# Optimization experiments

Hardware: AMD Instinct MI355X
Metric: run time of the kernel (lower is better)

Reference implementation:

```python
import jax, jax.numpy as jnp
import numpy as np

N, E, R, D = 100000, 600000, 3, 128  # nodes, edges per relation, relations, hidden


def setup_inputs() -> dict:
    key = jax.random.key(0)
    ks = jax.random.split(key, 12)
    sc = 1.0 / np.sqrt(D)
    return dict(
        x=jax.random.normal(ks[0], (N, D), jnp.float32),
        edge_src=jax.random.randint(ks[1], (R, E), 0, N, jnp.int32),
        edge_dst=jax.random.randint(ks[2], (R, E), 0, N, jnp.int32),
        edge_w=jax.random.uniform(ks[3], (R, E), jnp.float32),
        W=jax.random.normal(ks[4], (R, D, D), jnp.float32) * sc,
        attn_l=jax.random.normal(ks[5], (R, D), jnp.float32) * sc,
        attn_r=jax.random.normal(ks[6], (R, D), jnp.float32) * sc,
        gat_b=jnp.zeros((R, D), jnp.float32),
        bi_w=jax.random.normal(ks[7], (D, D), jnp.float32) * sc,
        bi_b=jnp.zeros((D,), jnp.float32),
        si_w=jax.random.normal(ks[8], (D, D), jnp.float32) * sc,
        si_b=jnp.zeros((D,), jnp.float32),
        res_w=jax.random.normal(ks[9], (), jnp.float32),
        ln_g=jnp.ones((D,), jnp.float32),
        ln_b=jnp.zeros((D,), jnp.float32),
    )


def _leaky(x, slope):
    return jnp.where(x >= 0, x, slope * x)


def _gat(x, W, al, ar, b, src, dst, ew):
    # DGL GATConv, 1 head, edge-weighted: h = xW; e = LReLU(a_l.h_src + a_r.h_dst);
    # alpha = edge_softmax(e per dst) * edge_weight; out[d] = sum alpha * h_src + bias.
    h = x @ W                                   # (N, D)
    el = (h * al).sum(-1)                       # (N,)
    er = (h * ar).sum(-1)                       # (N,)
    e = _leaky(el[src] + er[dst], 0.2)          # (E,)
    m = jax.ops.segment_max(e, dst, num_segments=N)
    a = jnp.exp(e - m[dst])
    s = jax.ops.segment_sum(a, dst, num_segments=N)
    alpha = a / s[dst] * ew                     # (E,)
    out = jax.ops.segment_sum(alpha[:, None] * h[src], dst, num_segments=N)
    return out + b                              # zero-indegree nodes -> bias only


def reference(x, edge_src, edge_dst, edge_w, W, attn_l, attn_r, gat_b,
              bi_w, bi_b, si_w, si_b, res_w, ln_g, ln_b):
    # per-relation intra aggregation, stacked along relation axis: (N, R, D)
    feats = jnp.stack(
        [_gat(x, W[r], attn_l[r], attn_r[r], gat_b[r],
              edge_src[r], edge_dst[r], edge_w[r]) for r in range(R)], axis=1)
    # FM-style bi-interaction over the relation axis
    s = feats.sum(axis=1)                       # (N, D)
    deep_fm = 0.5 * (s ** 2 - (feats ** 2).sum(axis=1))
    nfm = _leaky(deep_fm @ bi_w.T + bi_b, 0.01) + _leaky(s @ si_w.T + si_b, 0.01)
    # gated residual + LayerNorm
    out = nfm + x * jax.nn.sigmoid(res_w)
    mu = out.mean(-1, keepdims=True)
    var = ((out - mu) ** 2).mean(-1, keepdims=True)
    return (out - mu) * jax.lax.rsqrt(var + 1e-5) * ln_g + ln_b
```

## Files before the change

### kernel.cpp

```cpp
#include <hip/hip_runtime.h>

#define DD 128
typedef unsigned int u32;
typedef __attribute__((ext_vector_type(8))) short bf16x8;
typedef __attribute__((ext_vector_type(4))) float f32x4;

__device__ __forceinline__ float lrelu(float v, float s) { return v >= 0.f ? v : s * v; }
__device__ __forceinline__ ushort f2bf(float f) {
  union { float f; u32 u; } v; v.f = f;
  u32 u = v.u;
  return (ushort)((u + 0x7FFFu + ((u >> 16) & 1u)) >> 16);
}

union frag_cvt { uint4 u; bf16x8 h; };

__global__ __launch_bounds__(256) void k_prep_w(const float* __restrict__ W,
                                                short* __restrict__ WA)
{
  int t = blockIdx.x * 256 + threadIdx.x;
  int lane = t & 63, ks = (t >> 6) & 3, cf = (t >> 8) & 7, r = t >> 11;
  int c = cf * 16 + (lane & 15);
  int kb = ks * 32 + (lane >> 4) * 8;
  const float* Wr = W + (size_t)r * DD * DD;
  ushort o[8];
#pragma unroll
  for (int j = 0; j < 8; j++) o[j] = f2bf(Wr[(size_t)(kb + j) * DD + c]);
  uint4 st;
  st.x = (u32)o[0] | ((u32)o[1] << 16);
  st.y = (u32)o[2] | ((u32)o[3] << 16);
  st.z = (u32)o[4] | ((u32)o[5] << 16);
  st.w = (u32)o[6] | ((u32)o[7] << 16);
  *(uint4*)(WA + (size_t)t * 8) = st;
}

__global__ __launch_bounds__(256) void k_prep_cw(const float* __restrict__ bw,
                                                 const float* __restrict__ sw,
                                                 short* __restrict__ WB)
{
  int t = blockIdx.x * 256 + threadIdx.x;
  int lane = t & 63, ks = (t >> 6) & 3, cf = (t >> 8) & 7, m = t >> 11;
  const float* src = m ? sw : bw;
  int c = cf * 16 + (lane & 15);
  int k = ks * 32 + (lane >> 4) * 8;
  const float* pr = src + (size_t)c * DD + k;
  uint4 st;
  st.x = (u32)f2bf(pr[0]) | ((u32)f2bf(pr[1]) << 16);
  st.y = (u32)f2bf(pr[2]) | ((u32)f2bf(pr[3]) << 16);
  st.z = (u32)f2bf(pr[4]) | ((u32)f2bf(pr[5]) << 16);
  st.w = (u32)f2bf(pr[6]) | ((u32)f2bf(pr[7]) << 16);
  *(uint4*)(WB + (size_t)t * 8) = st;
}

__global__ void k_prep_av(const float* __restrict__ W, const float* __restrict__ al,
                          const float* __restrict__ ar, float* __restrict__ wl,
                          float* __restrict__ wr)
{
  int t = blockIdx.x * 192 + threadIdx.x;
  if (t >= 384) return;
  int r = t >> 7, k = t & 127;
  const float* Wrow = W + (size_t)r * DD * DD + (size_t)k * DD;
  const float* alr = al + r * DD;
  const float* arr = ar + r * DD;
  float pl = 0.f, pr = 0.f;
  for (int c = 0; c < DD; c++) { float w = Wrow[c]; pl = fmaf(w, alr[c], pl); pr = fmaf(w, arr[c], pr); }
  wl[t] = pl; wr[t] = pr;
}

__global__ __launch_bounds__(256) void k_prep_xrow(
    const float* __restrict__ x, const float* __restrict__ wl, const float* __restrict__ wr,
    u32* __restrict__ xrow, float* __restrict__ el, int2* __restrict__ bex, int N)
{
  const int wid = (int)(((long long)blockIdx.x * 256 + threadIdx.x) >> 6);
  const int lane = threadIdx.x & 63;
  if (wid >= N) return;
  float2 xv = *(const float2*)(x + (size_t)wid * DD + lane * 2);
  xrow[(size_t)wid * 64 + lane] = (u32)f2bf(xv.x) | ((u32)f2bf(xv.y) << 16);
  float d[6];
#pragma unroll
  for (int r = 0; r < 3; r++) {
    float2 wlv = *(const float2*)(wl + r * DD + lane * 2);
    float2 wrv = *(const float2*)(wr + r * DD + lane * 2);
    d[r]     = xv.x * wlv.x + xv.y * wlv.y;
    d[r + 3] = xv.x * wrv.x + xv.y * wrv.y;
  }
#pragma unroll
  for (int o = 32; o; o >>= 1) {
#pragma unroll
    for (int k = 0; k < 6; k++) d[k] += __shfl_xor(d[k], o);
  }
  if (lane == 0) {
#pragma unroll
    for (int r = 0; r < 3; r++) {
      el[(size_t)r * N + wid] = d[r];
      bex[(size_t)r * N + wid].y = __float_as_int(d[r + 3]);
    }
  }
}

__global__ void k_hist3(const int* __restrict__ dst, int* __restrict__ cnt,
                        int* __restrict__ rank, int N, int E) {
  int i = blockIdx.x * 256 + threadIdx.x;
  int r = blockIdx.y;
  if (i < E) {
    size_t ei = (size_t)r * E + i;
    rank[ei] = atomicAdd(cnt + (size_t)r * N + dst[ei], 1);
  }
}

__global__ __launch_bounds__(256) void k_scan_bsum(const int* __restrict__ cnt,
                                                   int* __restrict__ bsum, int M)
{
  __shared__ int red[256];
  const int t = threadIdx.x;
  const int g0 = blockIdx.x * 2048 + t * 8;
  int s = 0;
#pragma unroll
  for (int j = 0; j < 8; j++) { int i = g0 + j; if (i < M) s += cnt[i]; }
  red[t] = s;
  __syncthreads();
  for (int o = 128; o; o >>= 1) {
    if (t < o) red[t] += red[t + o];
    __syncthreads();
  }
  if (t == 0) bsum[blockIdx.x] = red[0];
}

__global__ __launch_bounds__(256) void k_scan_btop(const int* __restrict__ bsum,
                                                   int* __restrict__ bpre, int NB)
{
  __shared__ int sums[256];
  const int t = threadIdx.x;
  int v = (t < NB) ? bsum[t] : 0;
  sums[t] = v;
  __syncthreads();
  for (int o = 1; o < 256; o <<= 1) {
    int u = (t >= o) ? sums[t - o] : 0;
    __syncthreads();
    sums[t] += u;
    __syncthreads();
  }
  if (t < NB) bpre[t] = sums[t] - v;
}

__global__ __launch_bounds__(256) void k_scan_base(const int* __restrict__ cnt,
    const int* __restrict__ bpre, int2* __restrict__ bex, int M)
{
  __shared__ int sums[256];
  const int t = threadIdx.x;
  const int g0 = blockIdx.x * 2048 + t * 8;
  int c[8];
  int ts = 0;
#pragma unroll
  for (int j = 0; j < 8; j++) { int i = g0 + j; c[j] = (i < M) ? cnt[i] : 0; ts += c[j]; }
  sums[t] = ts;
  __syncthreads();
  for (int o = 1; o < 256; o <<= 1) {
    int u = (t >= o) ? sums[t - o] : 0;
    __syncthreads();
    sums[t] += u;
    __syncthreads();
  }
  int run = bpre[blockIdx.x] + sums[t] - ts;
#pragma unroll
  for (int j = 0; j < 8; j++) {
    int i = g0 + j;
    if (i <= M) bex[i].x = run;
    run += c[j];
  }
}

__global__ void k_scatter3(const int* __restrict__ src, const int* __restrict__ dst,
    const float* __restrict__ ew, const float* __restrict__ el,
    const int* __restrict__ rank, const int2* __restrict__ bex,
    int4* __restrict__ meta, int N, int E)
{
  int i = blockIdx.x * 256 + threadIdx.x;
  if (i >= E) return;
  int r = blockIdx.y;
  size_t ei = (size_t)r * E + i;
  int d = dst[ei], s = src[ei];
  int2 be = bex[(size_t)r * N + d];
  int pos = be.x + rank[ei];
  float e = lrelu(el[(size_t)r * N + s] + __int_as_float(be.y), 0.2f);
  meta[pos] = make_int4(s, __float_as_int(e), __float_as_int(ew[ei]), 0);
}

__global__ __launch_bounds__(256) void k_node_agg3(
    const int2* __restrict__ bex, const int4* __restrict__ meta,
    const u32* __restrict__ xrow, u32* __restrict__ aggx, int N, int Np)
{
  const int wid = (int)(((long long)blockIdx.x * 256 + threadIdx.x) >> 6);
  const int lane = threadIdx.x & 63;
  if (wid >= N) return;
  const char* xb = (const char*)xrow;
  const u32 lb = (u32)lane << 2;

  int b0[3], dg[3];
#pragma unroll
  for (int r = 0; r < 3; r++) {
    int v0 = bex[r * N + wid].x;
    int v1 = bex[r * N + wid + 1].x;
    b0[r] = v0; dg[r] = v1 - v0;
  }

  float A0[3] = {0.f, 0.f, 0.f}, A1[3] = {0.f, 0.f, 0.f}, SS[3];

  if (dg[0] <= 64 && dg[1] <= 64 && dg[2] <= 64) {
    int sv[3]; float av[3], cwv[3];
#pragma unroll
    for (int r = 0; r < 3; r++) {
      int s = 0; float a = 0.f, c = 0.f;
      if (lane < dg[r]) {
        int4 mm = meta[b0[r] + lane];
        s = mm.x;
        a = __expf(fminf(__int_as_float(mm.y), 60.f));
        c = a * __int_as_float(mm.z);
      }
      sv[r] = s; av[r] = a; cwv[r] = c;
    }
#pragma unroll
    for (int r = 0; r < 3; r++) {
      float s = av[r];
#pragma unroll
      for (int o = 32; o; o >>= 1) s += __shfl_xor(s, o);
      SS[r] = s;
    }
    float cc[3][8]; u32 oo[3][8];
#pragma unroll
    for (int r = 0; r < 3; r++)
#pragma unroll
      for (int q = 0; q < 8; q++) {
        cc[r][q] = __shfl(cwv[r], q);
        oo[r][q] = ((u32)__shfl(sv[r], q) << 8) | lb;
      }
    u32 uu[3][8];
#pragma unroll
    for (int r = 0; r < 3; r++)
#pragma unroll
      for (int q = 0; q < 8; q++) uu[r][q] = *(const u32*)(xb + oo[r][q]);
#pragma unroll
    for (int r = 0; r < 3; r++)
#pragma unroll
      for (int q = 0; q < 8; q++) {
        A0[r] = fmaf(cc[r][q], __uint_as_float(uu[r][q] << 16), A0[r]);
        A1[r] = fmaf(cc[r][q], __uint_as_float(uu[r][q] & 0xFFFF0000u), A1[r]);
      }
#pragma unroll
    for (int r = 0; r < 3; r++) {
      for (int c8 = 8; c8 < dg[r]; c8 += 8) {
        float c2[8]; u32 o2[8];
#pragma unroll
        for (int q = 0; q < 8; q++) {
          c2[q] = __shfl(cwv[r], c8 + q);
          o2[q] = ((u32)__shfl(sv[r], c8 + q) << 8) | lb;
        }
        u32 u2[8];
#pragma unroll
        for (int q = 0; q < 8; q++) u2[q] = *(const u32*)(xb + o2[q]);
#pragma unroll
        for (int q = 0; q < 8; q++) {
          A0[r] = fmaf(c2[q], __uint_as_float(u2[q] << 16), A0[r]);
          A1[r] = fmaf(c2[q], __uint_as_float(u2[q] & 0xFFFF0000u), A1[r]);
        }
      }
    }
  } else {
#pragma unroll
    for (int r = 0; r < 3; r++) {
      float sp = 0.f;
      for (int c0 = 0; c0 < dg[r]; c0 += 64) {
        int kk = min(64, dg[r] - c0);
        int s = 0; float a = 0.f, c = 0.f;
        if (lane < kk) {
          int4 mm = meta[b0[r] + c0 + lane];
          s = mm.x;
          a = __expf(fminf(__int_as_float(mm.y), 60.f));
          c = a * __int_as_float(mm.z);
        }
        sp += a;
        for (int c8 = 0; c8 < kk; c8 += 8) {
          float c2[8]; u32 o2[8];
#pragma unroll
          for (int q = 0; q < 8; q++) {
            c2[q] = __shfl(c, c8 + q);
            o2[q] = ((u32)__shfl(s, c8 + q) << 8) | lb;
          }
          u32 u2[8];
#pragma unroll
          for (int q = 0; q < 8; q++) u2[q] = *(const u32*)(xb + o2[q]);
#pragma unroll
          for (int q = 0; q < 8; q++) {
            A0[r] = fmaf(c2[q], __uint_as_float(u2[q] << 16), A0[r]);
            A1[r] = fmaf(c2[q], __uint_as_float(u2[q] & 0xFFFF0000u), A1[r]);
          }
        }
      }
#pragma unroll
      for (int o = 32; o; o >>= 1) sp += __shfl_xor(sp, o);
      SS[r] = sp;
    }
  }

#pragma unroll
  for (int r = 0; r < 3; r++) {
    const float inv = (dg[r] > 0) ? 1.f / SS[r] : 0.f;
    aggx[((size_t)r * Np + wid) * 64 + lane] =
        (u32)f2bf(A0[r] * inv) | ((u32)f2bf(A1[r] * inv) << 16);
  }
}

__global__ __launch_bounds__(512) void k_feats(
    const u32* __restrict__ aggx, const short* __restrict__ WA,
    const float* __restrict__ gb, u32* __restrict__ sfrag, u32* __restrict__ dfrag,
    int Np, int ntiles)
{
  extern __shared__ u32 ldsf[];
  u32* lwa = ldsf;
  const int tid = threadIdx.x;
  const int lane = tid & 63;
  const int w = tid >> 6;
  u32* wbuf = ldsf + 24576 + w * 1088;

  for (int i = tid; i < 6144; i += 512)
    *(uint4*)&lwa[i * 4] = *(const uint4*)(WA + (size_t)i * 8);
  __syncthreads();

  const int nl = lane & 15, fh = lane >> 4;

  for (int tile = blockIdx.x; tile < ntiles; tile += gridDim.x) {
    const int tb = tile * 128 + w * 16;
    const int nblk = tile * 8 + w;
    f32x4 sa[8], qa[8];
#pragma unroll
    for (int cf = 0; cf < 8; cf++) { sa[cf] = (f32x4){0,0,0,0}; qa[cf] = (f32x4){0,0,0,0}; }

    for (int r = 0; r < 3; r++) {
#pragma unroll
      for (int rr = 0; rr < 16; rr++)
        wbuf[rr * 68 + lane] = aggx[((size_t)r * Np + tb + rr) * 64 + lane];
      bf16x8 bf[4];
#pragma unroll
      for (int ks = 0; ks < 4; ks++) {
        frag_cvt cv;
        cv.u = *(const uint4*)&wbuf[nl * 68 + ks * 16 + fh * 4];
        bf[ks] = cv.h;
      }
      f32x4 acc[8];
#pragma unroll
      for (int cf = 0; cf < 8; cf++) acc[cf] = (f32x4){0,0,0,0};
#pragma unroll
      for (int ks = 0; ks < 4; ks++) {
#pragma unroll
        for (int cf = 0; cf < 8; cf++) {
          frag_cvt av;
          av.u = *(const uint4*)&lwa[(((r * 8 + cf) * 4 + ks) * 64 + lane) * 4];
          acc[cf] = __builtin_amdgcn_mfma_f32_16x16x32_bf16(av.h, bf[ks], acc[cf], 0, 0, 0);
        }
      }
#pragma unroll
      for (int cf = 0; cf < 8; cf++) {
        float4 g4 = *(const float4*)(gb + r * DD + cf * 16 + fh * 4);
        const float* gp = (const float*)&g4;
#pragma unroll
        for (int j = 0; j < 4; j++) {
          float f = acc[cf][j] + gp[j];
          sa[cf][j] += f;
          qa[cf][j] += f * f;
        }
      }
    }

#pragma unroll
    for (int cf = 0; cf < 8; cf++) {
      int wb = cf * 8 + fh * 2;
      wbuf[nl * 68 + wb]     = (u32)f2bf(sa[cf][0]) | ((u32)f2bf(sa[cf][1]) << 16);
      wbuf[nl * 68 + wb + 1] = (u32)f2bf(sa[cf][2]) | ((u32)f2bf(sa[cf][3]) << 16);
    }
#pragma unroll
    for (int ks = 0; ks < 4; ks++) {
      uint4 v = *(const uint4*)&wbuf[nl * 68 + ks * 16 + fh * 4];
      *(uint4*)&sfrag[(((size_t)nblk * 4 + ks) * 64 + lane) * 4] = v;
    }
#pragma unroll
    for (int cf = 0; cf < 8; cf++) {
      int wb = cf * 8 + fh * 2;
      float d0 = 0.5f * (sa[cf][0] * sa[cf][0] - qa[cf][0]);
      float d1 = 0.5f * (sa[cf][1] * sa[cf][1] - qa[cf][1]);
      float d2 = 0.5f * (sa[cf][2] * sa[cf][2] - qa[cf][2]);
      float d3 = 0.5f * (sa[cf][3] * sa[cf][3] - qa[cf][3]);
      wbuf[nl * 68 + wb]     = (u32)f2bf(d0) | ((u32)f2bf(d1) << 16);
      wbuf[nl * 68 + wb + 1] = (u32)f2bf(d2) | ((u32)f2bf(d3) << 16);
    }
#pragma unroll
    for (int ks = 0; ks < 4; ks++) {
      uint4 v = *(const uint4*)&wbuf[nl * 68 + ks * 16 + fh * 4];
      *(uint4*)&dfrag[(((size_t)nblk * 4 + ks) * 64 + lane) * 4] = v;
    }
  }
}

__global__ __launch_bounds__(512) void k_comb(
    const u32* __restrict__ sfrag, const u32* __restrict__ dfrag,
    const float* __restrict__ x, const short* __restrict__ WB,
    const float* __restrict__ bi_b, const float* __restrict__ si_b,
    const float* __restrict__ res_w, const float* __restrict__ ln_g,
    const float* __restrict__ ln_b, float* __restrict__ out, int N, int ntiles)
{
  extern __shared__ u32 ldsc[];
  u32* lwb = ldsc;
  const int tid = threadIdx.x;
  const int lane = tid & 63;
  const int w = tid >> 6;
  float* obuf = (float*)(ldsc + 16384) + w * 2112;

  for (int i = tid; i < 4096; i += 512)
    *(uint4*)&lwb[i * 4] = *(const uint4*)(WB + (size_t)i * 8);
  __syncthreads();

  const int nl = lane & 15, fh = lane >> 4;
  const float sigw = 1.f / (1.f + __expf(-res_w[0]));
  const float2 g2 = *(const float2*)(ln_g + lane * 2);
  const float2 b2 = *(const float2*)(ln_b + lane * 2);

  for (int tile = blockIdx.x; tile < ntiles; tile += gridDim.x) {
    const int tb = tile * 128 + w * 16;
    const int nblk = tile * 8 + w;
    const int node = tb + nl;

    bf16x8 sf[4], df[4];
#pragma unroll
    for (int ks = 0; ks < 4; ks++) {
      frag_cvt cs, cd;
      cs.u = *(const uint4*)&sfrag[(((size_t)nblk * 4 + ks) * 64 + lane) * 4];
      cd.u = *(const uint4*)&dfrag[(((size_t)nblk * 4 + ks) * 64 + lane) * 4];
      sf[ks] = cs.h; df[ks] = cd.h;
    }
    f32x4 accB[8], accS[8];
#pragma unroll
    for (int cf = 0; cf < 8; cf++) {
      accB[cf] = (f32x4){0,0,0,0};
      accS[cf] = (f32x4){0,0,0,0};
    }
#pragma unroll
    for (int ks = 0; ks < 4; ks++) {
#pragma unroll
      for (int cf = 0; cf < 8; cf++) {
        frag_cvt ab, as;
        ab.u = *(const uint4*)&lwb[(((0 * 8 + cf) * 4 + ks) * 64 + lane) * 4];
        as.u = *(const uint4*)&lwb[(((1 * 8 + cf) * 4 + ks) * 64 + lane) * 4];
        accB[cf] = __builtin_amdgcn_mfma_f32_16x16x32_bf16(ab.h, df[ks], accB[cf], 0, 0, 0);
        accS[cf] = __builtin_amdgcn_mfma_f32_16x16x32_bf16(as.h, sf[ks], accS[cf], 0, 0, 0);
      }
    }

    float sv = 0.f, sq = 0.f;
#pragma unroll
    for (int cf = 0; cf < 8; cf++) {
      int c0 = cf * 16 + fh * 4;
      float4 bb4 = *(const float4*)(bi_b + c0);
      float4 sb4 = *(const float4*)(si_b + c0);
      float4 xv = make_float4(0.f, 0.f, 0.f, 0.f);
      if (node < N) xv = *(const float4*)(x + (size_t)node * DD + c0);
      const float* bbp = (const float*)&bb4;
      const float* sbp = (const float*)&sb4;
      const float* xvp = (const float*)&xv;
      float4 o;
      float* op = (float*)&o;
#pragma unroll
      for (int j = 0; j < 4; j++) {
        float val = lrelu(accB[cf][j] + bbp[j], 0.01f)
                  + lrelu(accS[cf][j] + sbp[j], 0.01f)
                  + xvp[j] * sigw;
        op[j] = val;
        sv += val; sq += val * val;
      }
      *(float4*)&obuf[nl * 132 + c0] = o;
    }
    sv += __shfl_xor(sv, 16); sq += __shfl_xor(sq, 16);
    sv += __shfl_xor(sv, 32); sq += __shfl_xor(sq, 32);
    const float mu = sv * (1.f / DD);
    const float var = sq * (1.f / DD) - mu * mu;
    const float rs = rsqrtf(var + 1e-5f);

#pragma unroll
    for (int rr = 0; rr < 16; rr++) {
      int n2 = tb + rr;
      if (n2 >= N) continue;
      float mur = __shfl(mu, rr);
      float rsr = __shfl(rs, rr);
      float2 v = *(const float2*)&obuf[rr * 132 + lane * 2];
      float2 o;
      o.x = (v.x - mur) * rsr * g2.x + b2.x;
      o.y = (v.y - mur) * rsr * g2.y + b2.y;
      *(float2*)(out + (size_t)n2 * DD + lane * 2) = o;
    }
  }
}

extern "C" void kernel_launch(void* const* d_in, const int* in_sizes, int n_in,
                              void* d_out, int out_size, void* d_ws, size_t ws_size,
                              hipStream_t stream)
{
  const float* x    = (const float*)d_in[0];
  const int*   esrc = (const int*)d_in[1];
  const int*   edst = (const int*)d_in[2];
  const float* ew   = (const float*)d_in[3];
  const float* W    = (const float*)d_in[4];
  const float* al   = (const float*)d_in[5];
  const float* ar   = (const float*)d_in[6];
  const float* gb   = (const float*)d_in[7];
  const float* bi_w = (const float*)d_in[8];
  const float* bi_b = (const float*)d_in[9];
  const float* si_w = (const float*)d_in[10];
  const float* si_b = (const float*)d_in[11];
  const float* res_w= (const float*)d_in[12];
  const float* ln_g = (const float*)d_in[13];
  const float* ln_b = (const float*)d_in[14];

  const int N = in_sizes[0] / DD;
  const int R = 3;
  const int E = in_sizes[1] / R;
  const int Np = ((N + 127) / 128) * 128;
  const int M = R * N;
  const int NB = (M + 2047) / 2048;
  const int ntiles = Np / 128;

  auto al256 = [](size_t v) { return (v + 255) & ~(size_t)255; };
  char* p = (char*)d_ws;
  u32*   xrow  = (u32*)p;
  u32*   sfrag = (u32*)p;
  p += al256((size_t)Np * 64 * 4);
  int*   rank  = (int*)p;
  u32*   aggx  = (u32*)p;
  p += al256((size_t)R * Np * 64 * 4);
  int4*  meta  = (int4*)p;
  u32*   dfrag = (u32*)p;
  p += al256((size_t)R * E * 16);
  float* el    = (float*)p; p += al256((size_t)M * 4);
  int2*  bex   = (int2*)p;  p += al256(((size_t)M + 1) * 8);
  int*   cnt   = (int*)p;   p += al256((size_t)M * 4);
  short* WA    = (short*)p; p += al256((size_t)R * 8 * 4 * 64 * 8 * 2);
  short* WB    = (short*)p; p += al256((size_t)2 * 8 * 4 * 64 * 8 * 2);
  float* wl    = (float*)p; p += al256((size_t)R * DD * 4);
  float* wr    = (float*)p; p += al256((size_t)R * DD * 4);
  int*   bsum  = (int*)p;   p += 1024;
  int*   bpre  = (int*)p;   p += 1024;

  const int egrid = (E + 255) / 256;
  const int DYN_LDS = 133120;

  hipFuncSetAttribute((const void*)k_feats,
                      hipFuncAttributeMaxDynamicSharedMemorySize, DYN_LDS);
  hipFuncSetAttribute((const void*)k_comb,
                      hipFuncAttributeMaxDynamicSharedMemorySize, DYN_LDS);

  k_prep_w<<<24, 256, 0, stream>>>(W, WA);
  k_prep_cw<<<16, 256, 0, stream>>>(bi_w, si_w, WB);
  k_prep_av<<<2, 192, 0, stream>>>(W, al, ar, wl, wr);
  k_prep_xrow<<<(N + 3) / 4, 256, 0, stream>>>(x, wl, wr, xrow, el, bex, N);

  hipMemsetAsync(cnt, 0, (size_t)M * 4, stream);
  k_hist3<<<dim3(egrid, 3), 256, 0, stream>>>(edst, cnt, rank, N, E);
  k_scan_bsum<<<NB, 256, 0, stream>>>(cnt, bsum, M);
  k_scan_btop<<<1, 256, 0, stream>>>(bsum, bpre, NB);
  k_scan_base<<<NB, 256, 0, stream>>>(cnt, bpre, bex, M);
  k_scatter3<<<dim3(egrid, 3), 256, 0, stream>>>(esrc, edst, ew, el, rank, bex,
                                                 meta, N, E);
  k_node_agg3<<<(N + 3) / 4, 256, 0, stream>>>(bex, meta, xrow, aggx, N, Np);
  k_feats<<<256, 512, DYN_LDS, stream>>>(aggx, WA, gb, sfrag, dfrag, Np, ntiles);
  k_comb<<<256, 512, DYN_LDS, stream>>>(sfrag, dfrag, x, WB, bi_b, si_b,
                                        res_w, ln_g, ln_b, (float*)d_out, N, ntiles);
}
```

Before: 366.6 us.

## Pack edge metadata to 8 bytes and gather rows as 8-byte half-wave loads

Edge metadata shrinks from int4 (16 B) to int2, with the logit and edge weight stored as packed bf16. The node aggregation kernel now has each half-wave gather a full 256-byte bf16 row using 8-byte loads, so each load instruction serves two edges. The two halves are combined with a cross-lane shuffle, and half the lanes write the result. This cuts scatter and meta traffic and the number of gather instructions, but it adds bf16 rounding to the attention logits and weights, and dfrag now needs its own workspace region.

```diff
diff --git a/kernel.cpp b/kernel.cpp
--- a/kernel.cpp
+++ b/kernel.cpp
@@ -11,6 +11,7 @@
   u32 u = v.u;
   return (ushort)((u + 0x7FFFu + ((u >> 16) & 1u)) >> 16);
 }
+__device__ __forceinline__ float bf2f(ushort s) { return __uint_as_float(((u32)s) << 16); }
 
 union frag_cvt { uint4 u; bf16x8 h; };
 
@@ -172,7 +173,7 @@
 __global__ void k_scatter3(const int* __restrict__ src, const int* __restrict__ dst,
     const float* __restrict__ ew, const float* __restrict__ el,
     const int* __restrict__ rank, const int2* __restrict__ bex,
-    int4* __restrict__ meta, int N, int E)
+    int2* __restrict__ meta, int N, int E)
 {
   int i = blockIdx.x * 256 + threadIdx.x;
   if (i >= E) return;
@@ -182,18 +183,19 @@
   int2 be = bex[(size_t)r * N + d];
   int pos = be.x + rank[ei];
   float e = lrelu(el[(size_t)r * N + s] + __int_as_float(be.y), 0.2f);
-  meta[pos] = make_int4(s, __float_as_int(e), __float_as_int(ew[ei]), 0);
+  meta[pos] = make_int2(s, (int)((u32)f2bf(e) | ((u32)f2bf(ew[ei]) << 16)));
 }
 
 __global__ __launch_bounds__(256) void k_node_agg3(
-    const int2* __restrict__ bex, const int4* __restrict__ meta,
+    const int2* __restrict__ bex, const int2* __restrict__ meta,
     const u32* __restrict__ xrow, u32* __restrict__ aggx, int N, int Np)
 {
   const int wid = (int)(((long long)blockIdx.x * 256 + threadIdx.x) >> 6);
   const int lane = threadIdx.x & 63;
   if (wid >= N) return;
   const char* xb = (const char*)xrow;
-  const u32 lb = (u32)lane << 2;
+  const int ql = lane & 31, half = lane >> 5;
+  const u32 qb = (u32)ql << 3;
 
   int b0[3], dg[3];
 #pragma unroll
@@ -203,7 +205,7 @@
     b0[r] = v0; dg[r] = v1 - v0;
   }
 
-  float A0[3] = {0.f, 0.f, 0.f}, A1[3] = {0.f, 0.f, 0.f}, SS[3];
+  float A0[3] = {0,0,0}, A1[3] = {0,0,0}, A2[3] = {0,0,0}, A3[3] = {0,0,0}, SS[3];
 
   if (dg[0] <= 64 && dg[1] <= 64 && dg[2] <= 64) {
     int sv[3]; float av[3], cwv[3];
@@ -211,10 +213,12 @@
     for (int r = 0; r < 3; r++) {
       int s = 0; float a = 0.f, c = 0.f;
       if (lane < dg[r]) {
-        int4 mm = meta[b0[r] + lane];
+        int2 mm = meta[b0[r] + lane];
         s = mm.x;
-        a = __expf(fminf(__int_as_float(mm.y), 60.f));
-        c = a * __int_as_float(mm.z);
+        float e = bf2f((ushort)((u32)mm.y & 0xFFFFu));
+        float w = bf2f((ushort)((u32)mm.y >> 16));
+        a = __expf(fminf(e, 60.f));
+        c = a * w;
       }
       sv[r] = s; av[r] = a; cwv[r] = c;
     }
@@ -225,42 +229,48 @@
       for (int o = 32; o; o >>= 1) s += __shfl_xor(s, o);
       SS[r] = s;
     }
-    float cc[3][8]; u32 oo[3][8];
+    float cc[3][4]; u32 so[3][4];
 #pragma unroll
     for (int r = 0; r < 3; r++)
 #pragma unroll
-      for (int q = 0; q < 8; q++) {
-        cc[r][q] = __shfl(cwv[r], q);
-        oo[r][q] = ((u32)__shfl(sv[r], q) << 8) | lb;
-      }
-    u32 uu[3][8];
+      for (int q = 0; q < 4; q++) {
+        int j = q * 2 + half;
+        cc[r][q] = __shfl(cwv[r], j);
+        so[r][q] = ((u32)__shfl(sv[r], j) << 8) | qb;
+      }
+    uint2 uu[3][4];
 #pragma unroll
     for (int r = 0; r < 3; r++)
 #pragma unroll
-      for (int q = 0; q < 8; q++) uu[r][q] = *(const u32*)(xb + oo[r][q]);
+      for (int q = 0; q < 4; q++) uu[r][q] = *(const uint2*)(xb + so[r][q]);
 #pragma unroll
     for (int r = 0; r < 3; r++)
 #pragma unroll
-      for (int q = 0; q < 8; q++) {
-        A0[r] = fmaf(cc[r][q], __uint_as_float(uu[r][q] << 16), A0[r]);
-        A1[r] = fmaf(cc[r][q], __uint_as_float(uu[r][q] & 0xFFFF0000u), A1[r]);
+      for (int q = 0; q < 4; q++) {
+        A0[r] = fmaf(cc[r][q], __uint_as_float(uu[r][q].x << 16), A0[r]);
+        A1[r] = fmaf(cc[r][q], __uint_as_float(uu[r][q].x & 0xFFFF0000u), A1[r]);
+        A2[r] = fmaf(cc[r][q], __uint_as_float(uu[r][q].y << 16), A2[r]);
+        A3[r] = fmaf(cc[r][q], __uint_as_float(uu[r][q].y & 0xFFFF0000u), A3[r]);
       }
 #pragma unroll
     for (int r = 0; r < 3; r++) {
       for (int c8 = 8; c8 < dg[r]; c8 += 8) {
-        float c2[8]; u32 o2[8];
-#pragma unroll
-        for (int q = 0; q < 8; q++) {
-          c2[q] = __shfl(cwv[r], c8 + q);
-          o2[q] = ((u32)__shfl(sv[r], c8 + q) << 8) | lb;
+        float c2[4]; u32 o2[4];
+#pragma unroll
+        for (int q = 0; q < 4; q++) {
+          int j = c8 + q * 2 + half;
+          c2[q] = __shfl(cwv[r], j);
+          o2[q] = ((u32)__shfl(sv[r], j) << 8) | qb;
         }
-        u32 u2[8];
-#pragma unroll
-        for (int q = 0; q < 8; q++) u2[q] = *(const u32*)(xb + o2[q]);
-#pragma unroll
-        for (int q = 0; q < 8; q++) {
-          A0[r] = fmaf(c2[q], __uint_as_float(u2[q] << 16), A0[r]);
-          A1[r] = fmaf(c2[q], __uint_as_float(u2[q] & 0xFFFF0000u), A1[r]);
+        uint2 u2[4];
+#pragma unroll
+        for (int q = 0; q < 4; q++) u2[q] = *(const uint2*)(xb + o2[q]);
+#pragma unroll
+        for (int q = 0; q < 4; q++) {
+          A0[r] = fmaf(c2[q], __uint_as_float(u2[q].x << 16), A0[r]);
+          A1[r] = fmaf(c2[q], __uint_as_float(u2[q].x & 0xFFFF0000u), A1[r]);
+          A2[r] = fmaf(c2[q], __uint_as_float(u2[q].y << 16), A2[r]);
+          A3[r] = fmaf(c2[q], __uint_as_float(u2[q].y & 0xFFFF0000u), A3[r]);
         }
       }
     }
@@ -272,26 +282,31 @@
         int kk = min(64, dg[r] - c0);
         int s = 0; float a = 0.f, c = 0.f;
         if (lane < kk) {
-          int4 mm = meta[b0[r] + c0 + lane];
+          int2 mm = meta[b0[r] + c0 + lane];
           s = mm.x;
-          a = __expf(fminf(__int_as_float(mm.y), 60.f));
-          c = a * __int_as_float(mm.z);
+          float e = bf2f((ushort)((u32)mm.y & 0xFFFFu));
+          float w = bf2f((ushort)((u32)mm.y >> 16));
+          a = __expf(fminf(e, 60.f));
+          c = a * w;
         }
         sp += a;
         for (int c8 = 0; c8 < kk; c8 += 8) {
-          float c2[8]; u32 o2[8];
-#pragma unroll
-          for (int q = 0; q < 8; q++) {
-            c2[q] = __shfl(c, c8 + q);
-            o2[q] = ((u32)__shfl(s, c8 + q) << 8) | lb;
+          float c2[4]; u32 o2[4];
+#pragma unroll
+          for (int q = 0; q < 4; q++) {
+            int j = c8 + q * 2 + half;
+            c2[q] = __shfl(c, j);
+            o2[q] = ((u32)__shfl(s, j) << 8) | qb;
           }
-          u32 u2[8];
-#pragma unroll
-          for (int q = 0; q < 8; q++) u2[q] = *(const u32*)(xb + o2[q]);
-#pragma unroll
-          for (int q = 0; q < 8; q++) {
-            A0[r] = fmaf(c2[q], __uint_as_float(u2[q] << 16), A0[r]);
-            A1[r] = fmaf(c2[q], __uint_as_float(u2[q] & 0xFFFF0000u), A1[r]);
+          uint2 u2[4];
+#pragma unroll
+          for (int q = 0; q < 4; q++) u2[q] = *(const uint2*)(xb + o2[q]);
+#pragma unroll
+          for (int q = 0; q < 4; q++) {
+            A0[r] = fmaf(c2[q], __uint_as_float(u2[q].x << 16), A0[r]);
+            A1[r] = fmaf(c2[q], __uint_as_float(u2[q].x & 0xFFFF0000u), A1[r]);
+            A2[r] = fmaf(c2[q], __uint_as_float(u2[q].y << 16), A2[r]);
+            A3[r] = fmaf(c2[q], __uint_as_float(u2[q].y & 0xFFFF0000u), A3[r]);
           }
         }
       }
@@ -303,9 +318,20 @@
 
 #pragma unroll
   for (int r = 0; r < 3; r++) {
-    const float inv = (dg[r] > 0) ? 1.f / SS[r] : 0.f;
-    aggx[((size_t)r * Np + wid) * 64 + lane] =
-        (u32)f2bf(A0[r] * inv) | ((u32)f2bf(A1[r] * inv) << 16);
+    A0[r] += __shfl_xor(A0[r], 32);
+    A1[r] += __shfl_xor(A1[r], 32);
+    A2[r] += __shfl_xor(A2[r], 32);
+    A3[r] += __shfl_xor(A3[r], 32);
+  }
+  if (half == 0) {
+#pragma unroll
+    for (int r = 0; r < 3; r++) {
+      const float inv = (dg[r] > 0) ? 1.f / SS[r] : 0.f;
+      uint2 o;
+      o.x = (u32)f2bf(A0[r] * inv) | ((u32)f2bf(A1[r] * inv) << 16);
+      o.y = (u32)f2bf(A2[r] * inv) | ((u32)f2bf(A3[r] * inv) << 16);
+      *(uint2*)(aggx + ((size_t)r * Np + wid) * 64 + ql * 2) = o;
+    }
   }
 }
 
@@ -533,9 +559,8 @@
   int*   rank  = (int*)p;
   u32*   aggx  = (u32*)p;
   p += al256((size_t)R * Np * 64 * 4);
-  int4*  meta  = (int4*)p;
-  u32*   dfrag = (u32*)p;
-  p += al256((size_t)R * E * 16);
+  int2*  meta  = (int2*)p; p += al256((size_t)R * E * 8);
+  u32*   dfrag = (u32*)p;  p += al256((size_t)Np * 64 * 4);
   float* el    = (float*)p; p += al256((size_t)M * 4);
   int2*  bex   = (int2*)p;  p += al256(((size_t)M + 1) * 8);
   int*   cnt   = (int*)p;   p += al256((size_t)M * 4);
```

New measurement: 338.9 us. 1.08x faster.
